# Kernel optimization log

Hardware: AMD Instinct MI355X
Metric: run time of the kernel (lower is better)

## Reference

```python
import jax, jax.numpy as jnp
import numpy as np

B = 64          # batches
T = 65536       # total packed tokens
X = 512         # token feature dim
K = 5           # io pairs
Y = X * K       # extra dim = 2560
H = 512         # hidden


def setup_inputs() -> dict:
    key = jax.random.key(0)
    ks = jax.random.split(key, 13)
    s = 0.02  # weight scale
    return {
        "ps_data": jax.random.normal(ks[0], (T, X), jnp.float32),
        "io_embed": jax.random.normal(ks[1], (B, K, X), jnp.float32),
        "segment_ids": jnp.sort(jax.random.randint(ks[2], (T,), 0, B, dtype=jnp.int32)),
        # attention_fc: Linear(X+Y,512) -> ReLU -> Linear(512,512) -> ReLU -> Linear(512,1)
        "W1": jax.random.normal(ks[3], (X + Y, H), jnp.float32) * s,
        "b1": jnp.zeros((H,), jnp.float32),
        "W2": jax.random.normal(ks[4], (H, H), jnp.float32) * s,
        "b2": jnp.zeros((H,), jnp.float32),
        "W3": jax.random.normal(ks[5], (H, 1), jnp.float32) * s,
        "b3": jnp.zeros((1,), jnp.float32),
        # final_fc: Linear(512,512) -> ReLU -> Linear(512,2)
        "Wf1": jax.random.normal(ks[6], (H, H), jnp.float32) * s,
        "bf1": jnp.zeros((H,), jnp.float32),
        "Wf2": jax.random.normal(ks[7], (H, 2), jnp.float32) * s,
        "bf2": jnp.zeros((2,), jnp.float32),
    }


def reference(ps_data, io_embed, segment_ids, W1, b1, W2, b2, W3, b3, Wf1, bf1, Wf2, bf2):
    # io_embed (B,K,X) -> (B,Y); gather per token by its batch index
    extra = io_embed.reshape(B, -1)[segment_ids]            # (T, Y)
    h = jnp.concatenate([ps_data, extra], axis=1)           # (T, X+Y)
    h = jax.nn.relu(h @ W1 + b1)
    h = jax.nn.relu(h @ W2 + b2)
    logits = (h @ W3 + b3)[:, 0]                            # (T,)
    # per-segment softmax over ragged segments
    m = jax.lax.stop_gradient(
        jax.ops.segment_max(logits, segment_ids, num_segments=B))
    e = jnp.exp(logits - m[segment_ids])
    denom = jax.ops.segment_sum(e, segment_ids, num_segments=B)
    w = e / denom[segment_ids]                              # (T,)
    pooled = jax.ops.segment_sum(w[:, None] * ps_data, segment_ids,
                                 num_segments=B)            # (B, X)
    # final_fc
    return jax.nn.relu(pooled @ Wf1 + bf1) @ Wf2 + bf2      # (B, 2)
```

## Files before the change

kernel.cpp:

```cpp
#include <hip/hip_runtime.h>

#define T_TOK 65536
#define BATCH 64
#define XDIM  512
#define HDIM  512
#define YDIM  2560

#define BK 64
#define GM_TM 256
#define GM_TN 128

#define SB_KC 64
#define SB_KS 40
#define SB_BG 8

#define PREP_TRANS  2048
#define PREP_SB     320

typedef float  f32x4  __attribute__((ext_vector_type(4)));
typedef __bf16 bf16x8 __attribute__((ext_vector_type(8)));

__device__ __forceinline__ unsigned short f2bf(float f) {
    unsigned int u = __float_as_uint(f);
    return (unsigned short)((u + 0x7FFFu + ((u >> 16) & 1u)) >> 16);
}

__device__ __forceinline__ unsigned int pack_bf2(float hi, float lo) {
    return (__float_as_uint(hi) & 0xffff0000u) | (__float_as_uint(lo) >> 16);
}

__device__ __forceinline__ void load_lds16(const unsigned short* g, unsigned short* l) {
    __builtin_amdgcn_global_load_lds(
        (const __attribute__((address_space(1))) unsigned int*)g,
        (__attribute__((address_space(3))) unsigned int*)l, 16, 0, 0);
}

__device__ __forceinline__ int lower_bound_seg(const int* __restrict__ s, int n, int v) {
    int lo = 0, hi = n;
    while (lo < hi) { int mid = (lo + hi) >> 1; if (s[mid] < v) lo = mid + 1; else hi = mid; }
    return lo;
}

__global__ __launch_bounds__(256) void prep_kernel(const float* __restrict__ W1,
                                                   const float* __restrict__ W2,
                                                   unsigned short* __restrict__ w1t,
                                                   unsigned short* __restrict__ w2t,
                                                   const float* __restrict__ io,
                                                   float* __restrict__ partial) {
    __shared__ float sio[SB_BG][SB_KC];
    const int blk = blockIdx.x;
    const int t = threadIdx.x;

    if (blk < PREP_TRANS) {
        int bb = blk;
        const float* src = bb < 1024 ? W1 : W2;
        unsigned short* dst = bb < 1024 ? w1t : w2t;
        int idx = (bb & 1023) * 256 + t;
        int nn = idx >> 9, kk = idx & 511;
        dst[idx] = f2bf(src[(size_t)kk * 512 + nn]);
    } else {
        int sb = blk - PREP_TRANS;
        int s = sb >> 3, g = sb & 7;
        for (int i = t; i < SB_BG * SB_KC; i += 256) {
            int bb = i >> 6, kk = i & 63;
            sio[bb][kk] = io[(size_t)(g * SB_BG + bb) * YDIM + s * SB_KC + kk];
        }
        __syncthreads();
        float acc[SB_BG][2] = {};
        const int k0 = 512 + s * SB_KC;
        #pragma unroll 4
        for (int kk = 0; kk < SB_KC; kk++) {
            float wa = W1[(size_t)(k0 + kk) * 512 + t];
            float wb = W1[(size_t)(k0 + kk) * 512 + t + 256];
            #pragma unroll
            for (int bb = 0; bb < SB_BG; bb++) {
                acc[bb][0] += sio[bb][kk] * wa;
                acc[bb][1] += sio[bb][kk] * wb;
            }
        }
        #pragma unroll
        for (int bb = 0; bb < SB_BG; bb++) {
            int b = g * SB_BG + bb;
            partial[((size_t)s * BATCH + b) * 512 + t]       = acc[bb][0];
            partial[((size_t)s * BATCH + b) * 512 + t + 256] = acc[bb][1];
        }
    }
}

__global__ __launch_bounds__(256) void segbias_reduce(const float* __restrict__ partial,
                                                      float* __restrict__ segbias) {
    int idx = blockIdx.x * 256 + threadIdx.x;
    float s = 0.f;
    #pragma unroll
    for (int i = 0; i < SB_KS; i++) s += partial[(size_t)i * BATCH * 512 + idx];
    segbias[idx] = s;
}

#define FRAG_AT(sh, R, c) (*reinterpret_cast<const bf16x8*>(&(sh)[((R) * 8 + (((c) ^ ((R) & 7)))) * 8]))

__global__ __launch_bounds__(512) void gemm1_kernel(const float* __restrict__ ps,
                                                    const unsigned short* __restrict__ w1t,
                                                    const float* __restrict__ segbias,
                                                    const float* __restrict__ b1,
                                                    const int* __restrict__ segids,
                                                    unsigned short* __restrict__ h1) {
    __shared__ unsigned short shA[GM_TM * BK];
    __shared__ unsigned short shB[GM_TN * BK];

    const int bid = blockIdx.x;
    const int xcd = bid & 7;
    const int j = bid >> 3;
    const int n0 = (j & 3) * GM_TN;
    const int m0 = ((j >> 2) * 8 + xcd) * GM_TM;
    const int t = threadIdx.x;
    const int w = t >> 6, L = t & 63;
    const int mbase = (w >> 1) * 64, nbase = (w & 1) * 64;
    const int lrow = L & 15, lq = L >> 4;

    f32x4 acc[4][4] = {};

    for (int kt = 0; kt < XDIM; kt += BK) {
        #pragma unroll
        for (int i_ = 0; i_ < 2; i_++) {
            int g_ = i_ * 512 + t;
            int r_ = g_ >> 3, c_ = g_ & 7, cs_ = c_ ^ (r_ & 7);
            load_lds16(w1t + (size_t)(n0 + r_) * HDIM + kt + cs_ * 8, &shB[g_ * 8]);
        }
        #pragma unroll
        for (int i_ = 0; i_ < 4; i_++) {
            int g_ = i_ * 512 + t;
            int r_ = g_ >> 3, c_ = g_ & 7;
            const float4* s4 = reinterpret_cast<const float4*>(
                ps + (size_t)(m0 + r_) * XDIM + kt + c_ * 8);
            float4 x = s4[0], y = s4[1];
            uint4 pk;
            pk.x = pack_bf2(x.y, x.x);
            pk.y = pack_bf2(x.w, x.z);
            pk.z = pack_bf2(y.y, y.x);
            pk.w = pack_bf2(y.w, y.z);
            int cs_ = c_ ^ (r_ & 7);
            *reinterpret_cast<uint4*>(&shA[(r_ * 8 + cs_) * 8]) = pk;
        }
        __syncthreads();
        #pragma unroll
        for (int ks = 0; ks < BK; ks += 32) {
            bf16x8 af[4], bfr[4];
            #pragma unroll
            for (int i = 0; i < 4; i++) af[i] = FRAG_AT(shA, mbase + i * 16 + lrow, (ks >> 3) + lq);
            #pragma unroll
            for (int jj = 0; jj < 4; jj++) bfr[jj] = FRAG_AT(shB, nbase + jj * 16 + lrow, (ks >> 3) + lq);
            #pragma unroll
            for (int i = 0; i < 4; i++)
                #pragma unroll
                for (int jj = 0; jj < 4; jj++)
                    acc[i][jj] = __builtin_amdgcn_mfma_f32_16x16x32_bf16(af[i], bfr[jj], acc[i][jj], 0, 0, 0);
        }
        __syncthreads();
    }

    #pragma unroll
    for (int i = 0; i < 4; i++) {
        #pragma unroll
        for (int r = 0; r < 4; r++) {
            int gm = m0 + mbase + i * 16 + lq * 4 + r;
            int sg = segids[gm];
            const float* sb = segbias + (size_t)sg * HDIM;
            #pragma unroll
            for (int jj = 0; jj < 4; jj++) {
                int gn = n0 + nbase + jj * 16 + lrow;
                float v = acc[i][jj][r] + sb[gn] + b1[gn];
                v = v > 0.f ? v : 0.f;
                h1[(size_t)gm * HDIM + gn] = f2bf(v);
            }
        }
    }
}

__global__ __launch_bounds__(512) void gemm2_kernel(const unsigned short* __restrict__ h1,
                                                    const unsigned short* __restrict__ w2t,
                                                    const float* __restrict__ b2,
                                                    const float* __restrict__ w3,
                                                    float* __restrict__ logits8) {
    __shared__ unsigned short shA[GM_TM * BK];
    __shared__ unsigned short shB[GM_TN * BK];

    const int bid = blockIdx.x;
    const int xcd = bid & 7;
    const int j = bid >> 3;
    const int n0 = (j & 3) * GM_TN;
    const int m0 = ((j >> 2) * 8 + xcd) * GM_TM;
    const int t = threadIdx.x;
    const int w = t >> 6, L = t & 63;
    const int mbase = (w >> 1) * 64, nbase = (w & 1) * 64;
    const int lrow = L & 15, lq = L >> 4;

    f32x4 acc[4][4] = {};

    for (int kt = 0; kt < HDIM; kt += BK) {
        #pragma unroll
        for (int i_ = 0; i_ < 4; i_++) {
            int g_ = i_ * 512 + t;
            int r_ = g_ >> 3, c_ = g_ & 7, cs_ = c_ ^ (r_ & 7);
            load_lds16(h1 + (size_t)(m0 + r_) * HDIM + kt + cs_ * 8, &shA[g_ * 8]);
        }
        #pragma unroll
        for (int i_ = 0; i_ < 2; i_++) {
            int g_ = i_ * 512 + t;
            int r_ = g_ >> 3, c_ = g_ & 7, cs_ = c_ ^ (r_ & 7);
            load_lds16(w2t + (size_t)(n0 + r_) * HDIM + kt + cs_ * 8, &shB[g_ * 8]);
        }
        __syncthreads();
        #pragma unroll
        for (int ks = 0; ks < BK; ks += 32) {
            bf16x8 af[4], bfr[4];
            #pragma unroll
            for (int i = 0; i < 4; i++) af[i] = FRAG_AT(shA, mbase + i * 16 + lrow, (ks >> 3) + lq);
            #pragma unroll
            for (int jj = 0; jj < 4; jj++) bfr[jj] = FRAG_AT(shB, nbase + jj * 16 + lrow, (ks >> 3) + lq);
            #pragma unroll
            for (int i = 0; i < 4; i++)
                #pragma unroll
                for (int jj = 0; jj < 4; jj++)
                    acc[i][jj] = __builtin_amdgcn_mfma_f32_16x16x32_bf16(af[i], bfr[jj], acc[i][jj], 0, 0, 0);
        }
        __syncthreads();
    }

    float w3v[4], b2v[4];
    #pragma unroll
    for (int jj = 0; jj < 4; jj++) {
        int gn = n0 + nbase + jj * 16 + lrow;
        w3v[jj] = w3[gn];
        b2v[jj] = b2[gn];
    }
    const int slice = (j & 3) * 2 + (w & 1);
    #pragma unroll
    for (int i = 0; i < 4; i++) {
        #pragma unroll
        for (int r = 0; r < 4; r++) {
            float p = 0.f;
            #pragma unroll
            for (int jj = 0; jj < 4; jj++) {
                float h2 = acc[i][jj][r] + b2v[jj];
                h2 = h2 > 0.f ? h2 : 0.f;
                p += h2 * w3v[jj];
            }
            p += __shfl_xor(p, 1, 64);
            p += __shfl_xor(p, 2, 64);
            p += __shfl_xor(p, 4, 64);
            p += __shfl_xor(p, 8, 64);
            if (lrow == 0)
                logits8[(size_t)slice * T_TOK + m0 + mbase + i * 16 + lq * 4 + r] = p;
        }
    }
}

__global__ __launch_bounds__(512) void pool_kernel(const float* __restrict__ ps,
                                                   const float* __restrict__ logits8,
                                                   const int* __restrict__ segids,
                                                   float* __restrict__ pooled16) {
    const int s = blockIdx.x;
    const int b = blockIdx.y;
    const int t = threadIdx.x;
    __shared__ float wv[512];
    __shared__ float sred[8];
    const int start = lower_bound_seg(segids, T_TOK, b);
    const int end   = lower_bound_seg(segids, T_TOK, b + 1);

    float m = -3.4e38f;
    for (int i = start + t; i < end; i += 512) {
        float l = 0.f;
        #pragma unroll
        for (int k = 0; k < 8; k++) l += logits8[(size_t)k * T_TOK + i];
        m = fmaxf(m, l);
    }
    for (int d = 32; d; d >>= 1) m = fmaxf(m, __shfl_down(m, d, 64));
    if ((t & 63) == 0) sred[t >> 6] = m;
    __syncthreads();
    m = sred[0];
    #pragma unroll
    for (int k = 1; k < 8; k++) m = fmaxf(m, sred[k]);
    __syncthreads();
    float ss = 0.f;
    for (int i = start + t; i < end; i += 512) {
        float l = 0.f;
        #pragma unroll
        for (int k = 0; k < 8; k++) l += logits8[(size_t)k * T_TOK + i];
        ss += __expf(l - m);
    }
    for (int d = 32; d; d >>= 1) ss += __shfl_down(ss, d, 64);
    if ((t & 63) == 0) sred[t >> 6] = ss;
    __syncthreads();
    float denom = 0.f;
    #pragma unroll
    for (int k = 0; k < 8; k++) denom += sred[k];
    const float inv = 1.f / denom;

    const int n = end - start;
    const int per = (n + 15) >> 4;
    const int s0 = start + s * per;
    const int s1 = min(s0 + per, end);
    float acc = 0.f;
    for (int base = s0; base < s1; base += 512) {
        int cnt = min(512, s1 - base);
        __syncthreads();
        if (t < cnt) {
            float l = 0.f;
            #pragma unroll
            for (int k = 0; k < 8; k++) l += logits8[(size_t)k * T_TOK + base + t];
            wv[t] = __expf(l - m) * inv;
        }
        __syncthreads();
        for (int i = 0; i < cnt; i++)
            acc += wv[i] * ps[(size_t)(base + i) * XDIM + t];
    }
    pooled16[((size_t)s * BATCH + b) * XDIM + t] = acc;
}

__global__ __launch_bounds__(512) void final_kernel(const float* __restrict__ pooled16,
                                                    const float* __restrict__ wf1,
                                                    const float* __restrict__ bf1,
                                                    const float* __restrict__ wf2,
                                                    const float* __restrict__ bf2,
                                                    float* __restrict__ out) {
    const int b = blockIdx.x;
    const int t = threadIdx.x;
    __shared__ float sp[512];
    __shared__ float r0s[8], r1s[8];
    float pv = 0.f;
    #pragma unroll
    for (int k = 0; k < 16; k++) pv += pooled16[((size_t)k * BATCH + b) * XDIM + t];
    sp[t] = pv;
    __syncthreads();
    float acc = bf1[t];
    #pragma unroll 4
    for (int k = 0; k < 512; k++) acc += sp[k] * wf1[(size_t)k * 512 + t];
    float h = fmaxf(acc, 0.f);
    float p0 = h * wf2[t * 2 + 0];
    float p1 = h * wf2[t * 2 + 1];
    for (int d = 32; d; d >>= 1) { p0 += __shfl_down(p0, d, 64); p1 += __shfl_down(p1, d, 64); }
    if ((t & 63) == 0) { r0s[t >> 6] = p0; r1s[t >> 6] = p1; }
    __syncthreads();
    if (t == 0) {
        float a = 0.f, c = 0.f;
        #pragma unroll
        for (int i = 0; i < 8; i++) { a += r0s[i]; c += r1s[i]; }
        out[b * 2 + 0] = a + bf2[0];
        out[b * 2 + 1] = c + bf2[1];
    }
}

extern "C" void kernel_launch(void* const* d_in, const int* in_sizes, int n_in,
                              void* d_out, int out_size, void* d_ws, size_t ws_size,
                              hipStream_t stream) {
    const float* ps  = (const float*)d_in[0];
    const float* io  = (const float*)d_in[1];
    const int*   seg = (const int*)d_in[2];
    const float* W1  = (const float*)d_in[3];
    const float* b1  = (const float*)d_in[4];
    const float* W2  = (const float*)d_in[5];
    const float* b2  = (const float*)d_in[6];
    const float* W3  = (const float*)d_in[7];
    const float* Wf1 = (const float*)d_in[9];
    const float* bf1 = (const float*)d_in[10];
    const float* Wf2 = (const float*)d_in[11];
    const float* bf2 = (const float*)d_in[12];
    float* out = (float*)d_out;

    char* ws = (char*)d_ws;
    float*          segbias  = (float*)(ws + 0);
    unsigned short* w1t      = (unsigned short*)(ws + 131072);
    unsigned short* w2t      = (unsigned short*)(ws + 655360);
    float*          logits8  = (float*)(ws + 1179648);
    float*          pooled16 = (float*)(ws + 3276800);
    float*          partial  = (float*)(ws + 5373952);
    unsigned short* h1       = (unsigned short*)(ws + 16777216);

    prep_kernel<<<PREP_TRANS + PREP_SB, 256, 0, stream>>>(W1, W2, w1t, w2t, io, partial);
    segbias_reduce<<<128, 256, 0, stream>>>(partial, segbias);
    gemm1_kernel<<<(T_TOK / GM_TM) * 4, 512, 0, stream>>>(ps, w1t, segbias, b1, seg, h1);
    gemm2_kernel<<<(T_TOK / GM_TM) * 4, 512, 0, stream>>>(h1, w2t, b2, W3, logits8);
    pool_kernel<<<dim3(16, 64), 512, 0, stream>>>(ps, logits8, seg, pooled16);
    final_kernel<<<64, 512, 0, stream>>>(pooled16, Wf1, bf1, Wf2, bf2, out);
}
```

Baseline: 391.9 us.

## Pre-convert ps to bf16 once, load via LDS DMA, fold segbias reduce into atomics

A conversion phase added to the prep kernel writes ps as bf16. gemm1 then streams its A tile straight into LDS with global_load_lds instead of loading fp32 and packing in registers, and the pool kernel reads the half-size bf16 copy. The separate segbias reduction kernel is replaced by atomicAdd into a memset-zeroed buffer, which removes one launch. The cost is an extra full pass over ps (read fp32, write bf16) and atomic contention. Pooling now uses rounded bf16 activations, which slightly changes numerics.

Result: no change. 392.0 us (+0.0%).

```diff
diff --git a/kernel.cpp b/kernel.cpp
--- a/kernel.cpp
+++ b/kernel.cpp
@@ -14,6 +14,7 @@
 #define SB_KS 40
 #define SB_BG 8
 
+#define PREP_CONV   16384
 #define PREP_TRANS  2048
 #define PREP_SB     320
 
@@ -25,8 +26,8 @@
     return (unsigned short)((u + 0x7FFFu + ((u >> 16) & 1u)) >> 16);
 }
 
-__device__ __forceinline__ unsigned int pack_bf2(float hi, float lo) {
-    return (__float_as_uint(hi) & 0xffff0000u) | (__float_as_uint(lo) >> 16);
+__device__ __forceinline__ float bf2f(unsigned short u) {
+    return __uint_as_float((unsigned int)u << 16);
 }
 
 __device__ __forceinline__ void load_lds16(const unsigned short* g, unsigned short* l) {
@@ -41,25 +42,36 @@
     return lo;
 }
 
-__global__ __launch_bounds__(256) void prep_kernel(const float* __restrict__ W1,
+__global__ __launch_bounds__(256) void prep_kernel(const float* __restrict__ ps,
+                                                   unsigned short* __restrict__ psb,
+                                                   const float* __restrict__ W1,
                                                    const float* __restrict__ W2,
                                                    unsigned short* __restrict__ w1t,
                                                    unsigned short* __restrict__ w2t,
                                                    const float* __restrict__ io,
-                                                   float* __restrict__ partial) {
+                                                   float* __restrict__ segbias) {
     __shared__ float sio[SB_BG][SB_KC];
     const int blk = blockIdx.x;
     const int t = threadIdx.x;
 
-    if (blk < PREP_TRANS) {
-        int bb = blk;
+    if (blk < PREP_CONV) {
+        size_t idx = (size_t)blk * 256 + t;
+        const float4* s4 = reinterpret_cast<const float4*>(ps) + idx * 2;
+        float4 a = s4[0], b = s4[1];
+        ushort4 o0, o1;
+        o0.x = f2bf(a.x); o0.y = f2bf(a.y); o0.z = f2bf(a.z); o0.w = f2bf(a.w);
+        o1.x = f2bf(b.x); o1.y = f2bf(b.y); o1.z = f2bf(b.z); o1.w = f2bf(b.w);
+        reinterpret_cast<ushort4*>(psb)[idx * 2 + 0] = o0;
+        reinterpret_cast<ushort4*>(psb)[idx * 2 + 1] = o1;
+    } else if (blk < PREP_CONV + PREP_TRANS) {
+        int bb = blk - PREP_CONV;
         const float* src = bb < 1024 ? W1 : W2;
         unsigned short* dst = bb < 1024 ? w1t : w2t;
         int idx = (bb & 1023) * 256 + t;
         int nn = idx >> 9, kk = idx & 511;
         dst[idx] = f2bf(src[(size_t)kk * 512 + nn]);
     } else {
-        int sb = blk - PREP_TRANS;
+        int sb = blk - PREP_CONV - PREP_TRANS;
         int s = sb >> 3, g = sb & 7;
         for (int i = t; i < SB_BG * SB_KC; i += 256) {
             int bb = i >> 6, kk = i & 63;
@@ -81,24 +93,15 @@
         #pragma unroll
         for (int bb = 0; bb < SB_BG; bb++) {
             int b = g * SB_BG + bb;
-            partial[((size_t)s * BATCH + b) * 512 + t]       = acc[bb][0];
-            partial[((size_t)s * BATCH + b) * 512 + t + 256] = acc[bb][1];
-        }
-    }
-}
-
-__global__ __launch_bounds__(256) void segbias_reduce(const float* __restrict__ partial,
-                                                      float* __restrict__ segbias) {
-    int idx = blockIdx.x * 256 + threadIdx.x;
-    float s = 0.f;
-    #pragma unroll
-    for (int i = 0; i < SB_KS; i++) s += partial[(size_t)i * BATCH * 512 + idx];
-    segbias[idx] = s;
+            atomicAdd(&segbias[b * HDIM + t], acc[bb][0]);
+            atomicAdd(&segbias[b * HDIM + t + 256], acc[bb][1]);
+        }
+    }
 }
 
 #define FRAG_AT(sh, R, c) (*reinterpret_cast<const bf16x8*>(&(sh)[((R) * 8 + (((c) ^ ((R) & 7)))) * 8]))
 
-__global__ __launch_bounds__(512) void gemm1_kernel(const float* __restrict__ ps,
+__global__ __launch_bounds__(512) void gemm1_kernel(const unsigned short* __restrict__ psb,
                                                     const unsigned short* __restrict__ w1t,
                                                     const float* __restrict__ segbias,
                                                     const float* __restrict__ b1,
@@ -121,25 +124,16 @@
 
     for (int kt = 0; kt < XDIM; kt += BK) {
         #pragma unroll
+        for (int i_ = 0; i_ < 4; i_++) {
+            int g_ = i_ * 512 + t;
+            int r_ = g_ >> 3, c_ = g_ & 7, cs_ = c_ ^ (r_ & 7);
+            load_lds16(psb + (size_t)(m0 + r_) * XDIM + kt + cs_ * 8, &shA[g_ * 8]);
+        }
+        #pragma unroll
         for (int i_ = 0; i_ < 2; i_++) {
             int g_ = i_ * 512 + t;
             int r_ = g_ >> 3, c_ = g_ & 7, cs_ = c_ ^ (r_ & 7);
             load_lds16(w1t + (size_t)(n0 + r_) * HDIM + kt + cs_ * 8, &shB[g_ * 8]);
-        }
-        #pragma unroll
-        for (int i_ = 0; i_ < 4; i_++) {
-            int g_ = i_ * 512 + t;
-            int r_ = g_ >> 3, c_ = g_ & 7;
-            const float4* s4 = reinterpret_cast<const float4*>(
-                ps + (size_t)(m0 + r_) * XDIM + kt + c_ * 8);
-            float4 x = s4[0], y = s4[1];
-            uint4 pk;
-            pk.x = pack_bf2(x.y, x.x);
-            pk.y = pack_bf2(x.w, x.z);
-            pk.z = pack_bf2(y.y, y.x);
-            pk.w = pack_bf2(y.w, y.z);
-            int cs_ = c_ ^ (r_ & 7);
-            *reinterpret_cast<uint4*>(&shA[(r_ * 8 + cs_) * 8]) = pk;
         }
         __syncthreads();
         #pragma unroll
@@ -255,7 +249,7 @@
     }
 }
 
-__global__ __launch_bounds__(512) void pool_kernel(const float* __restrict__ ps,
+__global__ __launch_bounds__(512) void pool_kernel(const unsigned short* __restrict__ psb,
                                                    const float* __restrict__ logits8,
                                                    const int* __restrict__ segids,
                                                    float* __restrict__ pooled16) {
@@ -312,7 +306,7 @@
         }
         __syncthreads();
         for (int i = 0; i < cnt; i++)
-            acc += wv[i] * ps[(size_t)(base + i) * XDIM + t];
+            acc += wv[i] * bf2f(psb[(size_t)(base + i) * XDIM + t]);
     }
     pooled16[((size_t)s * BATCH + b) * XDIM + t] = acc;
 }
@@ -373,13 +367,15 @@
     unsigned short* w2t      = (unsigned short*)(ws + 655360);
     float*          logits8  = (float*)(ws + 1179648);
     float*          pooled16 = (float*)(ws + 3276800);
-    float*          partial  = (float*)(ws + 5373952);
-    unsigned short* h1       = (unsigned short*)(ws + 16777216);
-
-    prep_kernel<<<PREP_TRANS + PREP_SB, 256, 0, stream>>>(W1, W2, w1t, w2t, io, partial);
-    segbias_reduce<<<128, 256, 0, stream>>>(partial, segbias);
-    gemm1_kernel<<<(T_TOK / GM_TM) * 4, 512, 0, stream>>>(ps, w1t, segbias, b1, seg, h1);
+    unsigned short* psb      = (unsigned short*)(ws + 16777216);
+    unsigned short* h1       = (unsigned short*)(ws + 83886080);
+
+    hipMemsetAsync(ws, 0, 131072, stream);
+
+    prep_kernel<<<PREP_CONV + PREP_TRANS + PREP_SB, 256, 0, stream>>>(
+        ps, psb, W1, W2, w1t, w2t, io, segbias);
+    gemm1_kernel<<<(T_TOK / GM_TM) * 4, 512, 0, stream>>>(psb, w1t, segbias, b1, seg, h1);
     gemm2_kernel<<<(T_TOK / GM_TM) * 4, 512, 0, stream>>>(h1, w2t, b2, W3, logits8);
-    pool_kernel<<<dim3(16, 64), 512, 0, stream>>>(ps, logits8, seg, pooled16);
+    pool_kernel<<<dim3(16, 64), 512, 0, stream>>>(psb, logits8, seg, pooled16);
     final_kernel<<<64, 512, 0, stream>>>(pooled16, Wf1, bf1, Wf2, bf2, out);
 }
```
